# Performance work log

Measured on AMD Instinct MI355X. Metric: run time of the kernel, lower is better.

The kernel has to match this reference:

```python
import jax, jax.numpy as jnp
import numpy as np

B = 4096
OBS_DIM = 1024
E_OUT = 512
H1 = 2048
H2 = 2048


def setup_inputs() -> dict:
    key = jax.random.key(0)
    ks = jax.random.split(key, 12)
    def kaiming(k, shape, fan_in):
        return jax.random.normal(k, shape, dtype=jnp.float32) * np.float32(np.sqrt(2.0 / fan_in))
    obs = jax.random.normal(ks[0], (B, OBS_DIM), dtype=jnp.float32)
    # lineare: Linear(obs_dim, e_outputs), torch weight shape [out, in]
    We = kaiming(ks[1], (E_OUT, OBS_DIM), OBS_DIM)
    be = jax.random.normal(ks[2], (E_OUT,), dtype=jnp.float32) * 0.01
    # obs_dim attention heads, each Linear(e_outputs, 2), stacked
    attn_W = kaiming(ks[3], (OBS_DIM, E_OUT, 2), E_OUT)
    attn_b = jax.random.normal(ks[4], (OBS_DIM, 2), dtype=jnp.float32) * 0.01
    # v_net: Linear(obs_dim,H1)+tanh, Linear(H1,H2)+[dropout(eval:no-op)]+tanh, Linear(H2,1)
    W1 = kaiming(ks[5], (H1, OBS_DIM), OBS_DIM)
    b1 = jnp.zeros((H1,), dtype=jnp.float32)
    W2 = kaiming(ks[6], (H2, H1), H1)
    b2 = jnp.zeros((H2,), dtype=jnp.float32)
    W3 = kaiming(ks[7], (1, H2), H2)
    b3 = jnp.zeros((1,), dtype=jnp.float32)
    return {"obs": obs, "We": We, "be": be, "attn_W": attn_W, "attn_b": attn_b,
            "W1": W1, "b1": b1, "W2": W2, "b2": b2, "W3": W3, "b3": b3}


def reference(obs, We, be, attn_W, attn_b, W1, b1, W2, b2, W3, b3):
    # e = tanh(lineare(obs)) : [B, E_OUT]
    e = jnp.tanh(obs @ We.T + be)
    # all obs_dim attention heads batched into one contraction: [B, OBS_DIM, 2]
    logits = jnp.einsum('be,oec->boc', e, attn_W) + attn_b
    # softmax over the 2 logits, keep prob of class 1 -> Attention [B, OBS_DIM]
    attention = jax.nn.softmax(logits, axis=-1)[..., 1]
    state_attention = obs * attention
    # v_net (eval mode: dropout is identity)
    h = jnp.tanh(state_attention @ W1.T + b1)
    h = jnp.tanh(h @ W2.T + b2)
    v = jnp.squeeze(h @ W3.T + b3, -1)  # [B]
    return (v, attention)
```

## Files before the change

### kernel.cpp

```cpp
#include <hip/hip_runtime.h>
#include <hip/hip_bf16.h>

typedef unsigned short u16;
typedef u16 u16x4 __attribute__((ext_vector_type(4)));
typedef u16 u16x8 __attribute__((ext_vector_type(8)));
typedef __bf16 bf16x8 __attribute__((ext_vector_type(8)));
typedef float f32x4 __attribute__((ext_vector_type(4)));

__device__ __forceinline__ u16 f2bf(float f) {
  unsigned u = __float_as_uint(f);
  u += 0x7FFFu + ((u >> 16) & 1u);
  return (u16)(u >> 16);
}
__device__ __forceinline__ float bf2f(u16 h) {
  return __uint_as_float(((unsigned)h) << 16);
}
__device__ __forceinline__ float tanh_fast(float x) {
  float t = __expf(2.0f * x);
  return 1.0f - 2.0f / (t + 1.0f);
}
__device__ __forceinline__ float sigmoid_fast(float x) {
  return 1.0f / (1.0f + __expf(-x));
}

__device__ __forceinline__ void glds16(const u16* g, u16* l) {
  __builtin_amdgcn_global_load_lds(
      (const __attribute__((address_space(1))) unsigned int*)g,
      (__attribute__((address_space(3))) unsigned int*)l, 16, 0, 0);
}

__device__ __forceinline__ void cvt4(const float* __restrict__ s, u16* __restrict__ d, int q) {
  float4 v = ((const float4*)s)[q];
  u16x4 o = { f2bf(v.x), f2bf(v.y), f2bf(v.z), f2bf(v.w) };
  ((u16x4*)d)[q] = o;
}

__global__ __launch_bounds__(256)
void prep_kernel(const float* __restrict__ obs, const float* __restrict__ We,
                 const float* __restrict__ W1, const float* __restrict__ W2,
                 const float* __restrict__ aW, const float* __restrict__ ab,
                 u16* __restrict__ obs_b, u16* __restrict__ We_b,
                 u16* __restrict__ W1_b, u16* __restrict__ W2_b,
                 u16* __restrict__ Wd, float* __restrict__ bd,
                 float* __restrict__ vzero) {
  int q = blockIdx.x * 256 + threadIdx.x;
  if (q < 1024) ((float4*)vzero)[q] = (float4){0.f, 0.f, 0.f, 0.f};
  if (q < 1048576) { cvt4(obs, obs_b, q); return; }
  q -= 1048576;
  if (q < 131072) { cvt4(We, We_b, q); return; }
  q -= 131072;
  if (q < 524288) { cvt4(W1, W1_b, q); return; }
  q -= 524288;
  if (q < 1048576) { cvt4(W2, W2_b, q); return; }
  q -= 1048576;
  if (q < 131072) {
    int i0 = q * 4;
    int o = i0 >> 9, e0 = i0 & 511;
    const float* p = aW + (size_t)o * 1024 + e0 * 2;
    float4 v0 = *(const float4*)p;
    float4 v1 = *(const float4*)(p + 4);
    u16x4 od = { f2bf(v0.y - v0.x), f2bf(v0.w - v0.z),
                 f2bf(v1.y - v1.x), f2bf(v1.w - v1.z) };
    *(u16x4*)(Wd + i0) = od;
    if (q < 256) {
      float4 a0 = *(const float4*)(ab + q * 8);
      float4 a1 = *(const float4*)(ab + q * 8 + 4);
      float4 ob = { a0.y - a0.x, a0.w - a0.z, a1.y - a1.x, a1.w - a1.z };
      *(float4*)(bd + q * 4) = ob;
    }
  }
}

template <int BM, int BN, int EP>
__global__ __launch_bounds__(256, 2)
void gemm_bt(const u16* __restrict__ A, const u16* __restrict__ Bt,
             int N, int K,
             const float* __restrict__ bias,
             u16* __restrict__ outb, float* __restrict__ outf,
             const u16* __restrict__ obsb, u16* __restrict__ sa,
             const float* __restrict__ W3, const float* __restrict__ b3,
             float* __restrict__ vout) {
  constexpr int CA = BM / 32;
  constexpr int CB = BN / 32;
  constexpr int MI = BM / 32;
  constexpr int NJ = BN / 32;

  __shared__ __align__(16) u16 As0[BM * 64];
  __shared__ __align__(16) u16 Bs0[BN * 64];
  __shared__ __align__(16) u16 As1[BM * 64];
  __shared__ __align__(16) u16 Bs1[BN * 64];

  const int tid = threadIdx.x;
  const int lane = tid & 63;
  const int wave = tid >> 6;
  const int bm = blockIdx.x, bn = blockIdx.y;

  const int r0 = tid >> 3;
  const int kcs = ((tid & 7) ^ (r0 & 7)) * 8;

  const u16* gA = A + (size_t)(bm * BM + r0) * K + kcs;
  const u16* gB = Bt + (size_t)(bn * BN + r0) * K + kcs;

  const int wm = (wave >> 1) * (BM / 2);
  const int wn = (wave & 1) * (BN / 2);
  const int fr = lane & 15;
  const int hi = lane >> 4;
  const int frx = fr & 7;

  f32x4 acc[MI][NJ];
#pragma unroll
  for (int i = 0; i < MI; ++i)
#pragma unroll
    for (int j = 0; j < NJ; ++j)
      acc[i][j] = (f32x4){0.f, 0.f, 0.f, 0.f};

  auto stage = [&](u16* __restrict__ dA, u16* __restrict__ dB) {
#pragma unroll
    for (int q = 0; q < CA; ++q)
      glds16(gA + (size_t)q * 32 * K, dA + tid * 8 + q * 2048);
#pragma unroll
    for (int q = 0; q < CB; ++q)
      glds16(gB + (size_t)q * 32 * K, dB + tid * 8 + q * 2048);
    gA += 64; gB += 64;
  };

  auto compute = [&](const u16* sA, const u16* sB) {
#pragma unroll
    for (int s = 0; s < 2; ++s) {
      const int ck = ((s * 4 + hi) ^ frx) * 8;
      bf16x8 a[MI], b[NJ];
#pragma unroll
      for (int i = 0; i < MI; ++i)
        a[i] = *(const bf16x8*)(sA + (wm + i * 16 + fr) * 64 + ck);
#pragma unroll
      for (int j = 0; j < NJ; ++j)
        b[j] = *(const bf16x8*)(sB + (wn + j * 16 + fr) * 64 + ck);
#pragma unroll
      for (int i = 0; i < MI; ++i)
#pragma unroll
        for (int j = 0; j < NJ; ++j)
          acc[i][j] = __builtin_amdgcn_mfma_f32_16x16x32_bf16(a[i], b[j], acc[i][j], 0, 0, 0);
    }
  };

  const int T = K >> 6;
  stage(As0, Bs0);
  __syncthreads();
  for (int k = 0; k < T; k += 2) {
    stage(As1, Bs1);
    compute(As0, Bs0);
    __syncthreads();
    if (k + 2 < T) stage(As0, Bs0);
    compute(As1, Bs1);
    __syncthreads();
  }

  if constexpr (EP == 2) {
    float vpart[MI][4];
#pragma unroll
    for (int i = 0; i < MI; ++i)
#pragma unroll
      for (int r = 0; r < 4; ++r) vpart[i][r] = 0.f;
#pragma unroll
    for (int j = 0; j < NJ; ++j) {
      const int col = bn * BN + wn + j * 16 + fr;
      const float bv = bias[col];
      const float w3 = W3[col];
#pragma unroll
      for (int i = 0; i < MI; ++i)
#pragma unroll
        for (int r = 0; r < 4; ++r)
          vpart[i][r] += tanh_fast(acc[i][j][r] + bv) * w3;
    }
    const bool lead = (fr == 0);
    const bool addb = (bn == 0) && ((wave & 1) == 0);
#pragma unroll
    for (int i = 0; i < MI; ++i)
#pragma unroll
      for (int r = 0; r < 4; ++r) {
        float p = vpart[i][r];
        p += __shfl_xor(p, 8);
        p += __shfl_xor(p, 4);
        p += __shfl_xor(p, 2);
        p += __shfl_xor(p, 1);
        if (lead) {
          const int row = bm * BM + wm + i * 16 + (lane >> 4) * 4 + r;
          atomicAdd(vout + row, addb ? p + b3[0] : p);
        }
      }
  } else {
#pragma unroll
    for (int j = 0; j < NJ; ++j) {
      const int col = bn * BN + wn + j * 16 + fr;
      const float bv = bias[col];
#pragma unroll
      for (int i = 0; i < MI; ++i) {
#pragma unroll
        for (int r = 0; r < 4; ++r) {
          const int row = bm * BM + wm + i * 16 + (lane >> 4) * 4 + r;
          const float x = acc[i][j][r] + bv;
          const size_t idx = (size_t)row * N + col;
          if constexpr (EP == 0) {
            outb[idx] = f2bf(tanh_fast(x));
          } else {
            const float att = sigmoid_fast(x);
            outf[idx] = att;
            sa[idx] = f2bf(bf2f(obsb[idx]) * att);
          }
        }
      }
    }
  }
}

extern "C" void kernel_launch(void* const* d_in, const int* in_sizes, int n_in,
                              void* d_out, int out_size, void* d_ws, size_t ws_size,
                              hipStream_t stream) {
  const float* obs   = (const float*)d_in[0];
  const float* We    = (const float*)d_in[1];
  const float* be    = (const float*)d_in[2];
  const float* attnW = (const float*)d_in[3];
  const float* attnb = (const float*)d_in[4];
  const float* W1    = (const float*)d_in[5];
  const float* b1    = (const float*)d_in[6];
  const float* W2    = (const float*)d_in[7];
  const float* b2    = (const float*)d_in[8];
  const float* W3    = (const float*)d_in[9];
  const float* b3    = (const float*)d_in[10];
  float* out = (float*)d_out;

  char* ws = (char*)d_ws;
  u16*   We_b  = (u16*)(ws + 0x00000000);
  u16*   Wd_b  = (u16*)(ws + 0x00100000);
  u16*   W1_b  = (u16*)(ws + 0x00200000);
  u16*   W2_b  = (u16*)(ws + 0x00600000);
  float* bd    = (float*)(ws + 0x00E00000);
  u16*   obs_b = (u16*)(ws + 0x00E01000);
  u16*   e_b   = (u16*)(ws + 0x01601000);
  u16*   sa_b  = (u16*)(ws + 0x01A01000);
  u16*   h1_b  = (u16*)(ws + 0x02201000);

  prep_kernel<<<11264, 256, 0, stream>>>(obs, We, W1, W2, attnW, attnb,
                                         obs_b, We_b, W1_b, W2_b, Wd_b, bd, out);

  gemm_bt<64, 64, 0><<<dim3(64, 8), 256, 0, stream>>>(
      obs_b, We_b, 512, 1024, be, e_b, nullptr, nullptr, nullptr, nullptr, nullptr, nullptr);
  gemm_bt<128, 64, 1><<<dim3(32, 16), 256, 0, stream>>>(
      e_b, Wd_b, 1024, 512, bd, nullptr, out + 4096, obs_b, sa_b, nullptr, nullptr, nullptr);
  gemm_bt<128, 128, 0><<<dim3(32, 16), 256, 0, stream>>>(
      sa_b, W1_b, 2048, 1024, b1, h1_b, nullptr, nullptr, nullptr, nullptr, nullptr, nullptr);
  gemm_bt<128, 128, 2><<<dim3(32, 16), 256, 0, stream>>>(
      h1_b, W2_b, 2048, 2048, b2, nullptr, nullptr, nullptr, nullptr, W3, b3, out);
}
```

Before: 189.9 us.

## Overlap W1/W2 bf16 casts with earlier GEMMs via extra grid blocks

Removes the W1 and W2 fp32-to-bf16 conversions from the prep kernel and hands them to extra blocks appended to the grids of the first two GEMMs. Those blocks run a grid-stride cast loop while the real GEMM tiles compute, so the conversion bandwidth can overlap with compute. The prep kernel shrinks accordingly. The cast blocks compete with GEMM blocks for CUs and memory bandwidth, and ordering still holds because W1_b and W2_b are only consumed by later kernels on the same stream.

```diff
diff --git a/kernel.cpp b/kernel.cpp
--- a/kernel.cpp
+++ b/kernel.cpp
@@ -37,10 +37,8 @@
 
 __global__ __launch_bounds__(256)
 void prep_kernel(const float* __restrict__ obs, const float* __restrict__ We,
-                 const float* __restrict__ W1, const float* __restrict__ W2,
                  const float* __restrict__ aW, const float* __restrict__ ab,
                  u16* __restrict__ obs_b, u16* __restrict__ We_b,
-                 u16* __restrict__ W1_b, u16* __restrict__ W2_b,
                  u16* __restrict__ Wd, float* __restrict__ bd,
                  float* __restrict__ vzero) {
   int q = blockIdx.x * 256 + threadIdx.x;
@@ -49,10 +47,6 @@
   q -= 1048576;
   if (q < 131072) { cvt4(We, We_b, q); return; }
   q -= 131072;
-  if (q < 524288) { cvt4(W1, W1_b, q); return; }
-  q -= 524288;
-  if (q < 1048576) { cvt4(W2, W2_b, q); return; }
-  q -= 1048576;
   if (q < 131072) {
     int i0 = q * 4;
     int o = i0 >> 9, e0 = i0 & 511;
@@ -71,7 +65,7 @@
   }
 }
 
-template <int BM, int BN, int EP>
+template <int BM, int BN, int EP, int GYM, int CEX>
 __global__ __launch_bounds__(256, 2)
 void gemm_bt(const u16* __restrict__ A, const u16* __restrict__ Bt,
              int N, int K,
@@ -79,11 +73,22 @@
              u16* __restrict__ outb, float* __restrict__ outf,
              const u16* __restrict__ obsb, u16* __restrict__ sa,
              const float* __restrict__ W3, const float* __restrict__ b3,
-             float* __restrict__ vout) {
+             float* __restrict__ vout,
+             const float* __restrict__ castS, u16* __restrict__ castD, int castQ) {
   constexpr int CA = BM / 32;
   constexpr int CB = BN / 32;
   constexpr int MI = BM / 32;
   constexpr int NJ = BN / 32;
+
+  if constexpr (CEX > 0) {
+    if ((int)blockIdx.y >= GYM) {
+      const int idx = ((int)blockIdx.y - GYM) * (int)gridDim.x + (int)blockIdx.x;
+      const int stride = (int)gridDim.x * CEX * 256;
+      for (int q = idx * 256 + (int)threadIdx.x; q < castQ; q += stride)
+        cvt4(castS, castD, q);
+      return;
+    }
+  }
 
   __shared__ __align__(16) u16 As0[BM * 64];
   __shared__ __align__(16) u16 Bs0[BN * 64];
@@ -184,7 +189,7 @@
         p += __shfl_xor(p, 2);
         p += __shfl_xor(p, 1);
         if (lead) {
-          const int row = bm * BM + wm + i * 16 + (lane >> 4) * 4 + r;
+          const int row = bm * BM + wm + i * 16 + hi * 4 + r;
           atomicAdd(vout + row, addb ? p + b3[0] : p);
         }
       }
@@ -197,7 +202,7 @@
       for (int i = 0; i < MI; ++i) {
 #pragma unroll
         for (int r = 0; r < 4; ++r) {
-          const int row = bm * BM + wm + i * 16 + (lane >> 4) * 4 + r;
+          const int row = bm * BM + wm + i * 16 + hi * 4 + r;
           const float x = acc[i][j][r] + bv;
           const size_t idx = (size_t)row * N + col;
           if constexpr (EP == 0) {
@@ -240,15 +245,19 @@
   u16*   sa_b  = (u16*)(ws + 0x01A01000);
   u16*   h1_b  = (u16*)(ws + 0x02201000);
 
-  prep_kernel<<<11264, 256, 0, stream>>>(obs, We, W1, W2, attnW, attnb,
-                                         obs_b, We_b, W1_b, W2_b, Wd_b, bd, out);
-
-  gemm_bt<64, 64, 0><<<dim3(64, 8), 256, 0, stream>>>(
-      obs_b, We_b, 512, 1024, be, e_b, nullptr, nullptr, nullptr, nullptr, nullptr, nullptr);
-  gemm_bt<128, 64, 1><<<dim3(32, 16), 256, 0, stream>>>(
-      e_b, Wd_b, 1024, 512, bd, nullptr, out + 4096, obs_b, sa_b, nullptr, nullptr, nullptr);
-  gemm_bt<128, 128, 0><<<dim3(32, 16), 256, 0, stream>>>(
-      sa_b, W1_b, 2048, 1024, b1, h1_b, nullptr, nullptr, nullptr, nullptr, nullptr, nullptr);
-  gemm_bt<128, 128, 2><<<dim3(32, 16), 256, 0, stream>>>(
-      h1_b, W2_b, 2048, 2048, b2, nullptr, nullptr, nullptr, nullptr, W3, b3, out);
-}
+  prep_kernel<<<5120, 256, 0, stream>>>(obs, We, attnW, attnb,
+                                        obs_b, We_b, Wd_b, bd, out);
+
+  gemm_bt<64, 64, 0, 8, 2><<<dim3(64, 10), 256, 0, stream>>>(
+      obs_b, We_b, 512, 1024, be, e_b, nullptr, nullptr, nullptr,
+      nullptr, nullptr, nullptr, W1, W1_b, 524288);
+  gemm_bt<128, 64, 1, 16, 4><<<dim3(32, 20), 256, 0, stream>>>(
+      e_b, Wd_b, 1024, 512, bd, nullptr, out + 4096, obs_b, sa_b,
+      nullptr, nullptr, nullptr, W2, W2_b, 1048576);
+  gemm_bt<128, 128, 0, 16, 0><<<dim3(32, 16), 256, 0, stream>>>(
+      sa_b, W1_b, 2048, 1024, b1, h1_b, nullptr, nullptr, nullptr,
+      nullptr, nullptr, nullptr, nullptr, nullptr, 0);
+  gemm_bt<128, 128, 2, 16, 0><<<dim3(32, 16), 256, 0, stream>>>(
+      h1_b, W2_b, 2048, 2048, b2, nullptr, nullptr, nullptr, nullptr,
+      W3, b3, out, nullptr, nullptr, 0);
+}
```

New measurement: 193.6 us. Within noise of the previous version (+1.9%).
